# Kernel optimization log

Measured on AMD Instinct MI355X. Metric: run time of the kernel, lower is better.

## Reference

```python
import jax, jax.numpy as jnp
import numpy as np

N, E, B, D, H, C = 50000, 800000, 128, 64, 128, 2
EPS = 1e-5


def setup_inputs() -> dict:
    key = jax.random.key(0)
    ks = jax.random.split(key, 12)
    s = 0.1
    return {
        "x": jax.random.normal(ks[0], (N, D), jnp.float32),
        "edge_index": jax.random.randint(ks[1], (2, E), 0, N, jnp.int64),
        "batch": jnp.sort(jax.random.randint(ks[2], (N,), 0, B, jnp.int64)),
        "W_l": jax.random.normal(ks[3], (D, D), jnp.float32) * s,
        "b_l": jnp.zeros((D,), jnp.float32),
        "W_r": jax.random.normal(ks[4], (D, D), jnp.float32) * s,
        "W_res": jax.random.normal(ks[5], (D, D), jnp.float32) * s,
        "b_res": jnp.zeros((D,), jnp.float32),
        "gamma": jnp.ones((D,), jnp.float32),
        "beta": jnp.zeros((D,), jnp.float32),
        "gate_W1": jax.random.normal(ks[6], (D, D), jnp.float32) * s,
        "gate_b1": jnp.zeros((D,), jnp.float32),
        "gate_W2": jax.random.normal(ks[7], (D, 1), jnp.float32) * s,
        "gate_b2": jnp.zeros((1,), jnp.float32),
        "W_p1": jax.random.normal(ks[8], (D, H), jnp.float32) * s,
        "b_p1": jnp.zeros((H,), jnp.float32),
        "W_p2": jax.random.normal(ks[9], (H, C), jnp.float32) * s,
        "b_p2": jnp.zeros((C,), jnp.float32),
    }


def reference(x, edge_index, batch, W_l, b_l, W_r, W_res, b_res, gamma, beta,
              gate_W1, gate_b1, gate_W2, gate_b2, W_p1, b_p1, W_p2, b_p2):
    src, dst = edge_index[0], edge_index[1]
    # SAGEConv, mean aggregation: gather source feats, scatter-mean to target
    agg = jax.ops.segment_sum(x[src], dst, num_segments=N)          # [N, D]
    cnt = jax.ops.segment_sum(jnp.ones((E,), x.dtype), dst, num_segments=N)
    mean = agg / jnp.maximum(cnt, 1.0)[:, None]
    h = mean @ W_l + b_l + x @ W_r                                   # [N, D]
    # dropout is identity (eval mode)
    # BatchNorm1d (training-mode math: biased batch stats)
    mu = jnp.mean(h, axis=0)
    var = jnp.var(h, axis=0)
    h = (h - mu) * jax.lax.rsqrt(var + EPS) * gamma + beta
    # residual projection of the original features
    h = h + x @ W_res + b_res
    # GlobalAttention pooling: per-graph softmax over gate scores
    gate = jax.nn.relu(h @ gate_W1 + gate_b1) @ gate_W2 + gate_b2    # [N, 1]
    g = gate[:, 0]
    gmax = jax.ops.segment_max(g, batch, num_segments=B)
    gmax = jnp.where(jnp.isfinite(gmax), gmax, 0.0)
    e = jnp.exp(g - gmax[batch])
    z = jax.ops.segment_sum(e, batch, num_segments=B)
    alpha = e / jnp.maximum(z, 1e-16)[batch]
    pooled = jax.ops.segment_sum(alpha[:, None] * h, batch, num_segments=B)  # [B, D]
    # 2-layer predictor MLP with ReLU between
    out = jax.nn.relu(pooled @ W_p1 + b_p1) @ W_p2 + b_p2            # [B, C]
    return out
```

## Files before the change

kernel.cpp:

```cpp
#include <hip/hip_runtime.h>
#include <math.h>

#define N_NODES 50000
#define N_EDGES 800000
#define BATCHES 128
#define DIM 64
#define HID 128
#define NCLS 2
#define EPSV 1e-5f
#define MAXD 64

#define NPART 8
#define PART_SZ ((N_NODES + NPART - 1) / NPART)
#define EPB 2048
#define NCHK_E ((N_EDGES + EPB - 1) / EPB)
#define NCHUNK1 782

typedef __attribute__((ext_vector_type(8))) short bf16x8;
typedef __attribute__((ext_vector_type(4))) float f32x4;

__device__ __forceinline__ unsigned short f2bf(float f){
  unsigned u = __float_as_uint(f);
  u += 0x7FFFu + ((u >> 16) & 1u);
  return (unsigned short)(u >> 16);
}
__device__ __forceinline__ float bf2f(unsigned short h){
  return __uint_as_float(((unsigned)h) << 16);
}
__device__ __forceinline__ void split2(float f, unsigned short& hi, unsigned short& lo){
  hi = f2bf(f);
  lo = f2bf(f - bf2f(hi));
}
__device__ __forceinline__ uint4 pack8(const unsigned short* s){
  uint4 u;
  u.x = (unsigned)s[0] | ((unsigned)s[1] << 16);
  u.y = (unsigned)s[2] | ((unsigned)s[3] << 16);
  u.z = (unsigned)s[4] | ((unsigned)s[5] << 16);
  u.w = (unsigned)s[6] | ((unsigned)s[7] << 16);
  return u;
}

__global__ void k_scatter(const int* __restrict__ ei, int* __restrict__ cnt,
                          int* __restrict__ csr){
  const int p = blockIdx.x & (NPART-1);
  const int c = blockIdx.x >> 3;
  const int lo = p * PART_SZ;
  const int hi = lo + PART_SZ;
  const int e0 = c * EPB;
  const int e1 = (e0 + EPB < N_EDGES) ? e0 + EPB : N_EDGES;
  for (int i = e0 + threadIdx.x; i < e1; i += 256){
    int d = ei[N_EDGES + i];
    if (d >= lo && d < hi){
      int s = ei[i];
      int pos = atomicAdd(&cnt[d], 1);
      csr[(size_t)d*MAXD + pos] = s;
    }
  }
}

__global__ void k_mean(const float* __restrict__ x, const int* __restrict__ csr,
                       const int* __restrict__ cnt, float* __restrict__ meanb){
  const int node = (blockIdx.x*256 + threadIdx.x) >> 6;
  const int lane = threadIdx.x & 63;
  const int g = lane >> 4, f = lane & 15;
  const int dg = cnt[node];
  const int start = node * MAXD;
  float4 acc = make_float4(0.f,0.f,0.f,0.f);
  int e = (lane < dg) ? csr[start + lane] : 0;
  int i = 0;
  for (; i + 16 <= dg; i += 16){
    int s0 = __shfl(e, i +      g, 64);
    int s1 = __shfl(e, i + 4  + g, 64);
    int s2 = __shfl(e, i + 8  + g, 64);
    int s3 = __shfl(e, i + 12 + g, 64);
    float4 v0 = *(const float4*)&x[(size_t)s0*DIM + f*4];
    float4 v1 = *(const float4*)&x[(size_t)s1*DIM + f*4];
    float4 v2 = *(const float4*)&x[(size_t)s2*DIM + f*4];
    float4 v3 = *(const float4*)&x[(size_t)s3*DIM + f*4];
    acc.x += v0.x + v1.x + v2.x + v3.x;
    acc.y += v0.y + v1.y + v2.y + v3.y;
    acc.z += v0.z + v1.z + v2.z + v3.z;
    acc.w += v0.w + v1.w + v2.w + v3.w;
  }
  for (; i < dg; i += 4){
    int idx = i + g;
    int srcl = (idx < dg) ? idx : (dg - 1);
    int s = __shfl(e, srcl, 64);
    if (idx < dg){
      float4 v = *(const float4*)&x[(size_t)s*DIM + f*4];
      acc.x += v.x; acc.y += v.y; acc.z += v.z; acc.w += v.w;
    }
  }
  acc.x += __shfl_xor(acc.x, 16, 64); acc.x += __shfl_xor(acc.x, 32, 64);
  acc.y += __shfl_xor(acc.y, 16, 64); acc.y += __shfl_xor(acc.y, 32, 64);
  acc.z += __shfl_xor(acc.z, 16, 64); acc.z += __shfl_xor(acc.z, 32, 64);
  acc.w += __shfl_xor(acc.w, 16, 64); acc.w += __shfl_xor(acc.w, 32, 64);
  if (g == 0){
    float inv = 1.f / fmaxf((float)dg, 1.f);
    float4 r = make_float4(acc.x*inv, acc.y*inv, acc.z*inv, acc.w*inv);
    *(float4*)&meanb[(size_t)node*DIM + f*4] = r;
  }
}

__global__ void __launch_bounds__(256) k_lin1(
    const float* __restrict__ meanb, const float* __restrict__ x,
    const float* __restrict__ Wl, const float* __restrict__ bl,
    const float* __restrict__ Wr, float* __restrict__ hbuf,
    float* __restrict__ pstat){
  __shared__ __align__(16) short sB[2][64][136];
  __shared__ __align__(16) short sA[2][64][72];
  const int tid  = threadIdx.x;
  const int lane = tid & 63, w = tid >> 6;
  const int jc   = lane & 15;
  const int mrow = 16*w + jc;
  const int koff = (lane >> 4) * 8;
  const int r0   = 16*w + (lane >> 4)*4;
  const int base = blockIdx.x * 64;

  {
    const int k0 = 32 * w;
    #pragma unroll
    for (int kc = 0; kc < 4; ++kc){
      unsigned short h[8], l[8];
      #pragma unroll
      for (int i = 0; i < 8; ++i){
        int k = k0 + 8*kc + i;
        float v = (k < 64) ? Wl[k*DIM + lane] : Wr[(k-64)*DIM + lane];
        split2(v, h[i], l[i]);
      }
      *(uint4*)&sB[0][lane][k0 + 8*kc] = pack8(h);
      *(uint4*)&sB[1][lane][k0 + 8*kc] = pack8(l);
    }
  }

  float blv[4];
  #pragma unroll
  for (int nt = 0; nt < 4; ++nt) blv[nt] = bl[nt*16 + jc];

  f32x4 acc[4] = {};
  #pragma unroll
  for (int half = 0; half < 2; ++half){
    const float* __restrict__ src = half ? x : meanb;
    __syncthreads();
    {
      const int row = tid >> 2;
      const int kq  = (tid & 3) * 16;
      const int node = base + row;
      #pragma unroll
      for (int cc = 0; cc < 4; ++cc){
        float4 v = make_float4(0.f,0.f,0.f,0.f);
        if (node < N_NODES) v = *(const float4*)&src[(size_t)node*DIM + kq + 4*cc];
        unsigned short h[4], l[4];
        split2(v.x,h[0],l[0]); split2(v.y,h[1],l[1]);
        split2(v.z,h[2],l[2]); split2(v.w,h[3],l[3]);
        uint2 ph, pl;
        ph.x = (unsigned)h[0] | ((unsigned)h[1]<<16);
        ph.y = (unsigned)h[2] | ((unsigned)h[3]<<16);
        pl.x = (unsigned)l[0] | ((unsigned)l[1]<<16);
        pl.y = (unsigned)l[2] | ((unsigned)l[3]<<16);
        *(uint2*)&sA[0][row][kq + 4*cc] = ph;
        *(uint2*)&sA[1][row][kq + 4*cc] = pl;
      }
    }
    __syncthreads();
    #pragma unroll
    for (int kt2 = 0; kt2 < 2; ++kt2){
      const int ka = kt2*32 + koff;
      const int kb = half*64 + ka;
      bf16x8 ah = *(const bf16x8*)&sA[0][mrow][ka];
      bf16x8 al = *(const bf16x8*)&sA[1][mrow][ka];
      #pragma unroll
      for (int nt = 0; nt < 4; ++nt){
        const int nr = nt*16 + jc;
        bf16x8 bh = *(const bf16x8*)&sB[0][nr][kb];
        bf16x8 bo = *(const bf16x8*)&sB[1][nr][kb];
        acc[nt] = __builtin_amdgcn_mfma_f32_16x16x32_bf16(ah, bh, acc[nt], 0,0,0);
        acc[nt] = __builtin_amdgcn_mfma_f32_16x16x32_bf16(al, bh, acc[nt], 0,0,0);
        acc[nt] = __builtin_amdgcn_mfma_f32_16x16x32_bf16(ah, bo, acc[nt], 0,0,0);
      }
    }
  }

  float s1[4] = {0.f,0.f,0.f,0.f}, s2[4] = {0.f,0.f,0.f,0.f};
  #pragma unroll
  for (int nt = 0; nt < 4; ++nt){
    const int col = nt*16 + jc;
    #pragma unroll
    for (int r = 0; r < 4; ++r){
      const int node = base + r0 + r;
      float v = acc[nt][r] + blv[nt];
      if (node < N_NODES){
        hbuf[(size_t)node*DIM + col] = v;
        s1[nt] += v; s2[nt] += v*v;
      }
    }
  }

  __syncthreads();
  float* sred = (float*)sA;
  #pragma unroll
  for (int nt = 0; nt < 4; ++nt){
    float a = s1[nt], b = s2[nt];
    a += __shfl_xor(a, 16, 64); a += __shfl_xor(a, 32, 64);
    b += __shfl_xor(b, 16, 64); b += __shfl_xor(b, 32, 64);
    if ((lane >> 4) == 0){
      sred[0*256 + w*64 + nt*16 + jc] = a;
      sred[1*256 + w*64 + nt*16 + jc] = b;
    }
  }
  __syncthreads();
  if (tid < 64){
    float a = sred[tid] + sred[64+tid] + sred[128+tid] + sred[192+tid];
    float b = sred[256+tid] + sred[320+tid] + sred[384+tid] + sred[448+tid];
    pstat[(size_t)blockIdx.x*128 + tid]      = a;
    pstat[(size_t)blockIdx.x*128 + 64 + tid] = b;
  }
}

__global__ void __launch_bounds__(256) k_stats(
    const float* __restrict__ pstat, float* __restrict__ muinv){
  __shared__ float r1[256], r2[256];
  const int j = blockIdx.x;
  const int t = threadIdx.x;
  float s1 = 0.f, s2 = 0.f;
  for (int c = t; c < NCHUNK1; c += 256){
    s1 += pstat[(size_t)c*128 + j];
    s2 += pstat[(size_t)c*128 + 64 + j];
  }
  r1[t] = s1; r2[t] = s2;
  __syncthreads();
  for (int st = 128; st > 0; st >>= 1){
    if (t < st){ r1[t] += r1[t+st]; r2[t] += r2[t+st]; }
    __syncthreads();
  }
  if (t == 0){
    float mu = r1[0] / (float)N_NODES;
    float var = r2[0] / (float)N_NODES - mu*mu;
    muinv[j] = mu;
    muinv[DIM+j] = 1.0f / sqrtf(var + EPSV);
  }
}

__device__ __forceinline__ void stage_w64(short* sWh, short* sWl_,
                                          const float* __restrict__ W,
                                          int w, int lane){
  const int k0 = 16 * w;
  #pragma unroll
  for (int kc = 0; kc < 2; ++kc){
    unsigned short h[8], l[8];
    #pragma unroll
    for (int i = 0; i < 8; ++i){
      int k = k0 + 8*kc + i;
      split2(W[k*DIM + lane], h[i], l[i]);
    }
    *(uint4*)&sWh[lane*72 + k0 + 8*kc] = pack8(h);
    *(uint4*)&sWl_[lane*72 + k0 + 8*kc] = pack8(l);
  }
}

__global__ void __launch_bounds__(256) k_lin2(
    const float* __restrict__ x, float* __restrict__ hbuf,
    const float* __restrict__ Wres, const float* __restrict__ bres,
    const float* __restrict__ gamma, const float* __restrict__ beta,
    const float* __restrict__ muinv,
    const float* __restrict__ gW1, const float* __restrict__ gb1,
    const float* __restrict__ gW2, const float* __restrict__ gb2,
    float* __restrict__ gbuf){
  __shared__ __align__(16) short sW[2][64][72];
  __shared__ __align__(16) short sA[2][64][72];
  const int tid  = threadIdx.x;
  const int lane = tid & 63, w = tid >> 6;
  const int jc   = lane & 15;
  const int mrow = 16*w + jc;
  const int koff = (lane >> 4) * 8;
  const int r0   = 16*w + (lane >> 4)*4;
  const int base = blockIdx.x * 64;

  float muv[4], invv[4], gav[4], bev[4], brv[4], g1v[4], w2v[4];
  #pragma unroll
  for (int nt = 0; nt < 4; ++nt){
    const int col = nt*16 + jc;
    muv[nt] = muinv[col];  invv[nt] = muinv[DIM+col];
    gav[nt] = gamma[col];  bev[nt]  = beta[col];
    brv[nt] = bres[col];   g1v[nt]  = gb1[col];
    w2v[nt] = gW2[col];
  }
  const float gb2v = gb2[0];

  {
    const int row = tid >> 2;
    const int kq  = (tid & 3) * 16;
    const int node = base + row;
    #pragma unroll
    for (int cc = 0; cc < 4; ++cc){
      float4 v = make_float4(0.f,0.f,0.f,0.f);
      if (node < N_NODES) v = *(const float4*)&x[(size_t)node*DIM + kq + 4*cc];
      unsigned short h[4], l[4];
      split2(v.x,h[0],l[0]); split2(v.y,h[1],l[1]);
      split2(v.z,h[2],l[2]); split2(v.w,h[3],l[3]);
      uint2 ph, pl;
      ph.x = (unsigned)h[0] | ((unsigned)h[1]<<16);
      ph.y = (unsigned)h[2] | ((unsigned)h[3]<<16);
      pl.x = (unsigned)l[0] | ((unsigned)l[1]<<16);
      pl.y = (unsigned)l[2] | ((unsigned)l[3]<<16);
      *(uint2*)&sA[0][row][kq + 4*cc] = ph;
      *(uint2*)&sA[1][row][kq + 4*cc] = pl;
    }
  }
  stage_w64(&sW[0][0][0], &sW[1][0][0], Wres, w, lane);
  __syncthreads();

  f32x4 acc[4] = {};
  #pragma unroll
  for (int kt2 = 0; kt2 < 2; ++kt2){
    const int ka = kt2*32 + koff;
    bf16x8 ah = *(const bf16x8*)&sA[0][mrow][ka];
    bf16x8 al = *(const bf16x8*)&sA[1][mrow][ka];
    #pragma unroll
    for (int nt = 0; nt < 4; ++nt){
      const int nr = nt*16 + jc;
      bf16x8 bh = *(const bf16x8*)&sW[0][nr][ka];
      bf16x8 bo = *(const bf16x8*)&sW[1][nr][ka];
      acc[nt] = __builtin_amdgcn_mfma_f32_16x16x32_bf16(ah, bh, acc[nt], 0,0,0);
      acc[nt] = __builtin_amdgcn_mfma_f32_16x16x32_bf16(al, bh, acc[nt], 0,0,0);
      acc[nt] = __builtin_amdgcn_mfma_f32_16x16x32_bf16(ah, bo, acc[nt], 0,0,0);
    }
  }

  #pragma unroll
  for (int nt = 0; nt < 4; ++nt){
    const int col = nt*16 + jc;
    #pragma unroll
    for (int r = 0; r < 4; ++r){
      const int node = base + r0 + r;
      float hp = 0.f;
      if (node < N_NODES) hp = hbuf[(size_t)node*DIM + col];
      float v = (hp - muv[nt])*invv[nt]*gav[nt] + bev[nt] + brv[nt] + acc[nt][r];
      if (node < N_NODES) hbuf[(size_t)node*DIM + col] = v;
      unsigned short hh, ll;
      split2(v, hh, ll);
      sA[0][r0 + r][col] = (short)hh;
      sA[1][r0 + r][col] = (short)ll;
    }
  }
  __syncthreads();
  stage_w64(&sW[0][0][0], &sW[1][0][0], gW1, w, lane);
  __syncthreads();

  f32x4 acc2[4] = {};
  #pragma unroll
  for (int kt2 = 0; kt2 < 2; ++kt2){
    const int ka = kt2*32 + koff;
    bf16x8 ah = *(const bf16x8*)&sA[0][mrow][ka];
    bf16x8 al = *(const bf16x8*)&sA[1][mrow][ka];
    #pragma unroll
    for (int nt = 0; nt < 4; ++nt){
      const int nr = nt*16 + jc;
      bf16x8 bh = *(const bf16x8*)&sW[0][nr][ka];
      bf16x8 bo = *(const bf16x8*)&sW[1][nr][ka];
      acc2[nt] = __builtin_amdgcn_mfma_f32_16x16x32_bf16(ah, bh, acc2[nt], 0,0,0);
      acc2[nt] = __builtin_amdgcn_mfma_f32_16x16x32_bf16(al, bh, acc2[nt], 0,0,0);
      acc2[nt] = __builtin_amdgcn_mfma_f32_16x16x32_bf16(ah, bo, acc2[nt], 0,0,0);
    }
  }

  float p[4] = {0.f,0.f,0.f,0.f};
  #pragma unroll
  for (int nt = 0; nt < 4; ++nt){
    #pragma unroll
    for (int r = 0; r < 4; ++r)
      p[r] += fmaxf(acc2[nt][r] + g1v[nt], 0.f) * w2v[nt];
  }
  #pragma unroll
  for (int r = 0; r < 4; ++r){
    float t = p[r];
    t += __shfl_xor(t, 1, 64); t += __shfl_xor(t, 2, 64);
    t += __shfl_xor(t, 4, 64); t += __shfl_xor(t, 8, 64);
    const int node = base + r0 + r;
    if (jc == 0 && node < N_NODES){
      gbuf[node] = t + gb2v;
    }
  }
}

__global__ void __launch_bounds__(256) k_poolsum(
    const float* __restrict__ hbuf, const float* __restrict__ gbuf,
    const int* __restrict__ batch,
    float* __restrict__ zbuf, float* __restrict__ pooled){
  const int l = threadIdx.x >> 6, d = threadIdx.x & 63;
  const int i0 = blockIdx.x*64 + l*16;
  if (i0 >= N_NODES) return;
  int cur = batch[i0];
  float acc = 0.f, z = 0.f;
  const int iend = (i0 + 16 < N_NODES) ? i0 + 16 : N_NODES;
  for (int i = i0; i < iend; ++i){
    int b = batch[i];
    if (b != cur){
      atomicAdd(&pooled[cur*DIM + d], acc);
      if (d == 0) atomicAdd(&zbuf[cur], z);
      acc = 0.f; z = 0.f; cur = b;
    }
    float e = expf(gbuf[i]);
    z += e;
    acc += e * hbuf[(size_t)i*DIM + d];
  }
  atomicAdd(&pooled[cur*DIM + d], acc);
  if (d == 0) atomicAdd(&zbuf[cur], z);
}

__global__ void k_head(const float* __restrict__ pooled, const float* __restrict__ zbuf,
                       const float* __restrict__ Wp1, const float* __restrict__ bp1,
                       const float* __restrict__ Wp2, const float* __restrict__ bp2,
                       float* __restrict__ out){
  __shared__ float ps[DIM];
  __shared__ float red[4];
  int b = blockIdx.x;
  int t = threadIdx.x;
  if (t < DIM){
    float zz = fmaxf(zbuf[b], 1e-16f);
    ps[t] = pooled[b*DIM + t] / zz;
  }
  __syncthreads();
  float acc = bp1[t];
  #pragma unroll
  for (int d2=0; d2<DIM; d2++) acc = fmaf(ps[d2], Wp1[d2*HID + t], acc);
  acc = fmaxf(acc, 0.f);
  float o0 = acc * Wp2[t*NCLS+0];
  float o1 = acc * Wp2[t*NCLS+1];
  #pragma unroll
  for (int o=32;o>0;o>>=1){ o0 += __shfl_down(o0,o,64); o1 += __shfl_down(o1,o,64); }
  int w = t>>6;
  if ((t&63)==0){ red[w*2+0]=o0; red[w*2+1]=o1; }
  __syncthreads();
  if (t==0){
    out[b*NCLS+0] = red[0]+red[2]+bp2[0];
    out[b*NCLS+1] = red[1]+red[3]+bp2[1];
  }
}

extern "C" void kernel_launch(void* const* d_in, const int* in_sizes, int n_in,
                              void* d_out, int out_size, void* d_ws, size_t ws_size,
                              hipStream_t stream){
  const float* x     = (const float*)d_in[0];
  const int*   ei    = (const int*)d_in[1];
  const int*   batch = (const int*)d_in[2];
  const float* Wl    = (const float*)d_in[3];
  const float* bl    = (const float*)d_in[4];
  const float* Wr    = (const float*)d_in[5];
  const float* Wres  = (const float*)d_in[6];
  const float* bres  = (const float*)d_in[7];
  const float* gamma = (const float*)d_in[8];
  const float* beta  = (const float*)d_in[9];
  const float* gW1   = (const float*)d_in[10];
  const float* gb1   = (const float*)d_in[11];
  const float* gW2   = (const float*)d_in[12];
  const float* gb2   = (const float*)d_in[13];
  const float* Wp1   = (const float*)d_in[14];
  const float* bp1   = (const float*)d_in[15];
  const float* Wp2   = (const float*)d_in[16];
  const float* bp2   = (const float*)d_in[17];
  float* outp = (float*)d_out;

  int*   cnt   = (int*)d_ws;
  float* zbuf  = (float*)(cnt + N_NODES);
  float* pooled= zbuf + BATCHES;
  float* pstat = pooled + (size_t)BATCHES*DIM;
  float* muinv = pstat + (size_t)NCHUNK1*128;
  float* gbuf  = muinv + 2*DIM;
  float* meanb = gbuf + N_NODES;
  float* hbuf  = meanb + (size_t)N_NODES*DIM;
  int*   csr   = (int*)(hbuf + (size_t)N_NODES*DIM);

  const size_t zcount = (size_t)N_NODES + BATCHES + (size_t)BATCHES*DIM;
  hipMemsetAsync(d_ws, 0, zcount*sizeof(int), stream);

  k_scatter<<<NPART*NCHK_E, 256, 0, stream>>>(ei, cnt, csr);
  k_mean   <<<N_NODES/4, 256, 0, stream>>>(x, csr, cnt, meanb);
  k_lin1   <<<NCHUNK1, 256, 0, stream>>>(meanb, x, Wl, bl, Wr, hbuf, pstat);
  k_stats  <<<64, 256, 0, stream>>>(pstat, muinv);
  k_lin2   <<<NCHUNK1, 256, 0, stream>>>(x, hbuf, Wres, bres, gamma, beta, muinv,
                                         gW1, gb1, gW2, gb2, gbuf);
  k_poolsum<<<NCHUNK1, 256, 0, stream>>>(hbuf, gbuf, batch, zbuf, pooled);
  k_head   <<<BATCHES, HID, 0, stream>>>(pooled, zbuf, Wp1, bp1, Wp2, bp2, outp);
}
```

Measured before the change: 213.4 us.

## Fuse neighbor mean into lin1 and attention pooling into lin2, shrink CSR to u16

Computes neighbor means inside the first linear kernel directly into shared memory, removing the intermediate mean buffer and a launch. Attention pooling is folded into the second linear kernel: gate exponentials and per-graph segment sums are reduced in-block using a ballot mask of batch boundaries, then atomically added. This avoids writing h and gate scores back and rereading them. CSR indices are stored as 16-bit, which halves index traffic. The trade-off is that gather latency is now serialized per wave inside a GEMM block with lower occupancy.

```diff
diff --git a/kernel.cpp b/kernel.cpp
--- a/kernel.cpp
+++ b/kernel.cpp
@@ -41,7 +41,7 @@
 }
 
 __global__ void k_scatter(const int* __restrict__ ei, int* __restrict__ cnt,
-                          int* __restrict__ csr){
+                          unsigned short* __restrict__ csr){
   const int p = blockIdx.x & (NPART-1);
   const int c = blockIdx.x >> 3;
   const int lo = p * PART_SZ;
@@ -53,57 +53,14 @@
     if (d >= lo && d < hi){
       int s = ei[i];
       int pos = atomicAdd(&cnt[d], 1);
-      csr[(size_t)d*MAXD + pos] = s;
-    }
-  }
-}
-
-__global__ void k_mean(const float* __restrict__ x, const int* __restrict__ csr,
-                       const int* __restrict__ cnt, float* __restrict__ meanb){
-  const int node = (blockIdx.x*256 + threadIdx.x) >> 6;
-  const int lane = threadIdx.x & 63;
-  const int g = lane >> 4, f = lane & 15;
-  const int dg = cnt[node];
-  const int start = node * MAXD;
-  float4 acc = make_float4(0.f,0.f,0.f,0.f);
-  int e = (lane < dg) ? csr[start + lane] : 0;
-  int i = 0;
-  for (; i + 16 <= dg; i += 16){
-    int s0 = __shfl(e, i +      g, 64);
-    int s1 = __shfl(e, i + 4  + g, 64);
-    int s2 = __shfl(e, i + 8  + g, 64);
-    int s3 = __shfl(e, i + 12 + g, 64);
-    float4 v0 = *(const float4*)&x[(size_t)s0*DIM + f*4];
-    float4 v1 = *(const float4*)&x[(size_t)s1*DIM + f*4];
-    float4 v2 = *(const float4*)&x[(size_t)s2*DIM + f*4];
-    float4 v3 = *(const float4*)&x[(size_t)s3*DIM + f*4];
-    acc.x += v0.x + v1.x + v2.x + v3.x;
-    acc.y += v0.y + v1.y + v2.y + v3.y;
-    acc.z += v0.z + v1.z + v2.z + v3.z;
-    acc.w += v0.w + v1.w + v2.w + v3.w;
-  }
-  for (; i < dg; i += 4){
-    int idx = i + g;
-    int srcl = (idx < dg) ? idx : (dg - 1);
-    int s = __shfl(e, srcl, 64);
-    if (idx < dg){
-      float4 v = *(const float4*)&x[(size_t)s*DIM + f*4];
-      acc.x += v.x; acc.y += v.y; acc.z += v.z; acc.w += v.w;
-    }
-  }
-  acc.x += __shfl_xor(acc.x, 16, 64); acc.x += __shfl_xor(acc.x, 32, 64);
-  acc.y += __shfl_xor(acc.y, 16, 64); acc.y += __shfl_xor(acc.y, 32, 64);
-  acc.z += __shfl_xor(acc.z, 16, 64); acc.z += __shfl_xor(acc.z, 32, 64);
-  acc.w += __shfl_xor(acc.w, 16, 64); acc.w += __shfl_xor(acc.w, 32, 64);
-  if (g == 0){
-    float inv = 1.f / fmaxf((float)dg, 1.f);
-    float4 r = make_float4(acc.x*inv, acc.y*inv, acc.z*inv, acc.w*inv);
-    *(float4*)&meanb[(size_t)node*DIM + f*4] = r;
+      csr[(size_t)d*MAXD + pos] = (unsigned short)s;
+    }
   }
 }
 
 __global__ void __launch_bounds__(256) k_lin1(
-    const float* __restrict__ meanb, const float* __restrict__ x,
+    const float* __restrict__ x, const unsigned short* __restrict__ csr,
+    const int* __restrict__ cnt,
     const float* __restrict__ Wl, const float* __restrict__ bl,
     const float* __restrict__ Wr, float* __restrict__ hbuf,
     float* __restrict__ pstat){
@@ -111,6 +68,7 @@
   __shared__ __align__(16) short sA[2][64][72];
   const int tid  = threadIdx.x;
   const int lane = tid & 63, w = tid >> 6;
+  const int g    = lane >> 4, f = lane & 15;
   const int jc   = lane & 15;
   const int mrow = 16*w + jc;
   const int koff = (lane >> 4) * 8;
@@ -132,6 +90,7 @@
       *(uint4*)&sB[1][lane][k0 + 8*kc] = pack8(l);
     }
   }
+  __syncthreads();
 
   float blv[4];
   #pragma unroll
@@ -140,16 +99,63 @@
   f32x4 acc[4] = {};
   #pragma unroll
   for (int half = 0; half < 2; ++half){
-    const float* __restrict__ src = half ? x : meanb;
-    __syncthreads();
-    {
-      const int row = tid >> 2;
-      const int kq  = (tid & 3) * 16;
-      const int node = base + row;
+    if (half == 0){
+      for (int n = 0; n < 16; ++n){
+        const int node = base + 16*w + n;
+        int dg = 0;
+        if (node < N_NODES) dg = cnt[node];
+        const size_t start = (size_t)node * MAXD;
+        int e = (lane < dg) ? (int)csr[start + lane] : 0;
+        float4 a4 = make_float4(0.f,0.f,0.f,0.f);
+        int i = 0;
+        for (; i + 16 <= dg; i += 16){
+          int s0 = __shfl(e, i +      g, 64);
+          int s1 = __shfl(e, i + 4  + g, 64);
+          int s2 = __shfl(e, i + 8  + g, 64);
+          int s3 = __shfl(e, i + 12 + g, 64);
+          float4 v0 = *(const float4*)&x[(size_t)s0*DIM + f*4];
+          float4 v1 = *(const float4*)&x[(size_t)s1*DIM + f*4];
+          float4 v2 = *(const float4*)&x[(size_t)s2*DIM + f*4];
+          float4 v3 = *(const float4*)&x[(size_t)s3*DIM + f*4];
+          a4.x += v0.x + v1.x + v2.x + v3.x;
+          a4.y += v0.y + v1.y + v2.y + v3.y;
+          a4.z += v0.z + v1.z + v2.z + v3.z;
+          a4.w += v0.w + v1.w + v2.w + v3.w;
+        }
+        for (; i < dg; i += 4){
+          int idx = i + g;
+          int srcl = (idx < dg) ? idx : (dg - 1);
+          int s = __shfl(e, srcl, 64);
+          if (idx < dg){
+            float4 v = *(const float4*)&x[(size_t)s*DIM + f*4];
+            a4.x += v.x; a4.y += v.y; a4.z += v.z; a4.w += v.w;
+          }
+        }
+        a4.x += __shfl_xor(a4.x, 16, 64); a4.x += __shfl_xor(a4.x, 32, 64);
+        a4.y += __shfl_xor(a4.y, 16, 64); a4.y += __shfl_xor(a4.y, 32, 64);
+        a4.z += __shfl_xor(a4.z, 16, 64); a4.z += __shfl_xor(a4.z, 32, 64);
+        a4.w += __shfl_xor(a4.w, 16, 64); a4.w += __shfl_xor(a4.w, 32, 64);
+        if (g == 0){
+          float inv = 1.f / fmaxf((float)dg, 1.f);
+          unsigned short h[4], l[4];
+          split2(a4.x*inv,h[0],l[0]); split2(a4.y*inv,h[1],l[1]);
+          split2(a4.z*inv,h[2],l[2]); split2(a4.w*inv,h[3],l[3]);
+          uint2 ph, pl;
+          ph.x = (unsigned)h[0] | ((unsigned)h[1]<<16);
+          ph.y = (unsigned)h[2] | ((unsigned)h[3]<<16);
+          pl.x = (unsigned)l[0] | ((unsigned)l[1]<<16);
+          pl.y = (unsigned)l[2] | ((unsigned)l[3]<<16);
+          *(uint2*)&sA[0][16*w + n][f*4] = ph;
+          *(uint2*)&sA[1][16*w + n][f*4] = pl;
+        }
+      }
+    } else {
       #pragma unroll
-      for (int cc = 0; cc < 4; ++cc){
+      for (int s4 = 0; s4 < 4; ++s4){
+        const int row = 16*w + s4*4 + g;
+        const int node = base + row;
         float4 v = make_float4(0.f,0.f,0.f,0.f);
-        if (node < N_NODES) v = *(const float4*)&src[(size_t)node*DIM + kq + 4*cc];
+        if (node < N_NODES) v = *(const float4*)&x[(size_t)node*DIM + f*4];
         unsigned short h[4], l[4];
         split2(v.x,h[0],l[0]); split2(v.y,h[1],l[1]);
         split2(v.z,h[2],l[2]); split2(v.w,h[3],l[3]);
@@ -158,11 +164,10 @@
         ph.y = (unsigned)h[2] | ((unsigned)h[3]<<16);
         pl.x = (unsigned)l[0] | ((unsigned)l[1]<<16);
         pl.y = (unsigned)l[2] | ((unsigned)l[3]<<16);
-        *(uint2*)&sA[0][row][kq + 4*cc] = ph;
-        *(uint2*)&sA[1][row][kq + 4*cc] = pl;
+        *(uint2*)&sA[0][row][f*4] = ph;
+        *(uint2*)&sA[1][row][f*4] = pl;
       }
     }
-    __syncthreads();
     #pragma unroll
     for (int kt2 = 0; kt2 < 2; ++kt2){
       const int ka = kt2*32 + koff;
@@ -259,18 +264,22 @@
 }
 
 __global__ void __launch_bounds__(256) k_lin2(
-    const float* __restrict__ x, float* __restrict__ hbuf,
+    const float* __restrict__ x, const float* __restrict__ hbuf,
     const float* __restrict__ Wres, const float* __restrict__ bres,
     const float* __restrict__ gamma, const float* __restrict__ beta,
     const float* __restrict__ muinv,
     const float* __restrict__ gW1, const float* __restrict__ gb1,
     const float* __restrict__ gW2, const float* __restrict__ gb2,
-    float* __restrict__ gbuf){
+    const int* __restrict__ batch,
+    float* __restrict__ zbuf, float* __restrict__ pooled){
   __shared__ __align__(16) short sW[2][64][72];
   __shared__ __align__(16) short sA[2][64][72];
+  __shared__ int sb[64];
+  __shared__ unsigned long long runmask;
   const int tid  = threadIdx.x;
   const int lane = tid & 63, w = tid >> 6;
   const int jc   = lane & 15;
+  const int g16  = w*4 + (lane >> 4);
   const int mrow = 16*w + jc;
   const int koff = (lane >> 4) * 8;
   const int r0   = 16*w + (lane >> 4)*4;
@@ -307,8 +316,18 @@
       *(uint2*)&sA[1][row][kq + 4*cc] = pl;
     }
   }
+  if (tid < 64){
+    int nn = base + tid;
+    sb[tid] = batch[(nn < N_NODES) ? nn : (N_NODES-1)];
+  }
   stage_w64(&sW[0][0][0], &sW[1][0][0], Wres, w, lane);
   __syncthreads();
+
+  if (w == 0){
+    bool fl = (lane > 0) && (sb[lane] != sb[lane-1]);
+    unsigned long long mm = __ballot(fl);
+    if (lane == 0) runmask = mm;
+  }
 
   f32x4 acc[4] = {};
   #pragma unroll
@@ -327,6 +346,7 @@
     }
   }
 
+  float vk[4][4];
   #pragma unroll
   for (int nt = 0; nt < 4; ++nt){
     const int col = nt*16 + jc;
@@ -336,7 +356,7 @@
       float hp = 0.f;
       if (node < N_NODES) hp = hbuf[(size_t)node*DIM + col];
       float v = (hp - muv[nt])*invv[nt]*gav[nt] + bev[nt] + brv[nt] + acc[nt][r];
-      if (node < N_NODES) hbuf[(size_t)node*DIM + col] = v;
+      vk[nt][r] = v;
       unsigned short hh, ll;
       split2(v, hh, ll);
       sA[0][r0 + r][col] = (short)hh;
@@ -371,41 +391,54 @@
     for (int r = 0; r < 4; ++r)
       p[r] += fmaxf(acc2[nt][r] + g1v[nt], 0.f) * w2v[nt];
   }
+  float ev[4];
   #pragma unroll
   for (int r = 0; r < 4; ++r){
     float t = p[r];
     t += __shfl_xor(t, 1, 64); t += __shfl_xor(t, 2, 64);
     t += __shfl_xor(t, 4, 64); t += __shfl_xor(t, 8, 64);
     const int node = base + r0 + r;
-    if (jc == 0 && node < N_NODES){
-      gbuf[node] = t + gb2v;
-    }
-  }
-}
-
-__global__ void __launch_bounds__(256) k_poolsum(
-    const float* __restrict__ hbuf, const float* __restrict__ gbuf,
-    const int* __restrict__ batch,
-    float* __restrict__ zbuf, float* __restrict__ pooled){
-  const int l = threadIdx.x >> 6, d = threadIdx.x & 63;
-  const int i0 = blockIdx.x*64 + l*16;
-  if (i0 >= N_NODES) return;
-  int cur = batch[i0];
-  float acc = 0.f, z = 0.f;
-  const int iend = (i0 + 16 < N_NODES) ? i0 + 16 : N_NODES;
-  for (int i = i0; i < iend; ++i){
-    int b = batch[i];
-    if (b != cur){
-      atomicAdd(&pooled[cur*DIM + d], acc);
-      if (d == 0) atomicAdd(&zbuf[cur], z);
-      acc = 0.f; z = 0.f; cur = b;
-    }
-    float e = expf(gbuf[i]);
-    z += e;
-    acc += e * hbuf[(size_t)i*DIM + d];
-  }
-  atomicAdd(&pooled[cur*DIM + d], acc);
-  if (d == 0) atomicAdd(&zbuf[cur], z);
+    ev[r] = (node < N_NODES) ? expf(t + gb2v) : 0.f;
+  }
+
+  float* sredp = (float*)&sW[0][0][0];
+  float* szl   = sredp + 16*64;
+  __syncthreads();
+  const unsigned long long m = runmask;
+  int rstart = 0;
+  while (rstart < 64){
+    const int bseg = sb[rstart];
+    unsigned long long rest = (rstart >= 63) ? 0ull : (m >> (rstart+1));
+    const int rend = rest ? (rstart + 1 + __builtin_ctzll(rest)) : 64;
+    float pacc[4] = {0.f,0.f,0.f,0.f};
+    float zacc = 0.f;
+    #pragma unroll
+    for (int r = 0; r < 4; ++r){
+      const int ln = 4*g16 + r;
+      if (ln >= rstart && ln < rend){
+        #pragma unroll
+        for (int nt = 0; nt < 4; ++nt) pacc[nt] += ev[r]*vk[nt][r];
+        zacc += ev[r];
+      }
+    }
+    #pragma unroll
+    for (int nt = 0; nt < 4; ++nt) sredp[g16*64 + nt*16 + jc] = pacc[nt];
+    if ((lane & 15) == 0) szl[g16] = zacc;
+    __syncthreads();
+    if (tid < 64){
+      float s = 0.f;
+      #pragma unroll 4
+      for (int g2 = 0; g2 < 16; ++g2) s += sredp[g2*64 + tid];
+      atomicAdd(&pooled[bseg*DIM + tid], s);
+    }
+    if (tid == 64){
+      float sz2 = 0.f;
+      for (int g2 = 0; g2 < 16; ++g2) sz2 += szl[g2];
+      atomicAdd(&zbuf[bseg], sz2);
+    }
+    __syncthreads();
+    rstart = rend;
+  }
 }
 
 __global__ void k_head(const float* __restrict__ pooled, const float* __restrict__ zbuf,
@@ -466,20 +499,16 @@
   float* pooled= zbuf + BATCHES;
   float* pstat = pooled + (size_t)BATCHES*DIM;
   float* muinv = pstat + (size_t)NCHUNK1*128;
-  float* gbuf  = muinv + 2*DIM;
-  float* meanb = gbuf + N_NODES;
-  float* hbuf  = meanb + (size_t)N_NODES*DIM;
-  int*   csr   = (int*)(hbuf + (size_t)N_NODES*DIM);
+  float* hbuf  = muinv + 2*DIM;
+  unsigned short* csr = (unsigned short*)(hbuf + (size_t)N_NODES*DIM);
 
   const size_t zcount = (size_t)N_NODES + BATCHES + (size_t)BATCHES*DIM;
   hipMemsetAsync(d_ws, 0, zcount*sizeof(int), stream);
 
   k_scatter<<<NPART*NCHK_E, 256, 0, stream>>>(ei, cnt, csr);
-  k_mean   <<<N_NODES/4, 256, 0, stream>>>(x, csr, cnt, meanb);
-  k_lin1   <<<NCHUNK1, 256, 0, stream>>>(meanb, x, Wl, bl, Wr, hbuf, pstat);
+  k_lin1   <<<NCHUNK1, 256, 0, stream>>>(x, csr, cnt, Wl, bl, Wr, hbuf, pstat);
   k_stats  <<<64, 256, 0, stream>>>(pstat, muinv);
   k_lin2   <<<NCHUNK1, 256, 0, stream>>>(x, hbuf, Wres, bres, gamma, beta, muinv,
-                                         gW1, gb1, gW2, gb2, gbuf);
-  k_poolsum<<<NCHUNK1, 256, 0, stream>>>(hbuf, gbuf, batch, zbuf, pooled);
+                                         gW1, gb1, gW2, gb2, batch, zbuf, pooled);
   k_head   <<<BATCHES, HID, 0, stream>>>(pooled, zbuf, Wp1, bp1, Wp2, bp2, outp);
 }
```

Result: slower. 231.1 us (+8.3%).
